# Performance work log

Measured on AMD Instinct MI355X. Metric: run time of the kernel, lower is better.

Reference implementation:

```python
import math
import jax, jax.numpy as jnp
import numpy as np

B, N, C, H = 64, 197, 768, 12
KEEP_RATE = 0.7

def setup_inputs() -> dict:
    key = jax.random.key(0)
    k0, k1, k2 = jax.random.split(key, 3)
    x = jax.random.normal(k0, (B, N, C), jnp.float32)
    qkv_w = jax.random.normal(k1, (C, 3 * C), jnp.float32) * 0.02
    qkv_b = jnp.zeros((3 * C,), jnp.float32)
    proj_w = jax.random.normal(k2, (C, C), jnp.float32) * 0.02
    proj_b = jnp.zeros((C,), jnp.float32)
    return {"x": x, "qkv_w": qkv_w, "qkv_b": qkv_b, "proj_w": proj_w, "proj_b": proj_b}

def reference(x, qkv_w, qkv_b, proj_w, proj_b):
    b, n, c = x.shape
    d = c // H
    scale = d ** -0.5
    # qkv: [B,N,3C] -> [3,B,H,N,d]
    qkv = (x @ qkv_w + qkv_b).reshape(b, n, 3, H, d)
    qkv = jnp.transpose(qkv, (2, 0, 3, 1, 4))
    q, k, v = qkv[0], qkv[1], qkv[2]
    attn = jax.nn.softmax(jnp.einsum('bhnd,bhmd->bhnm', q, k) * scale, axis=-1)  # [B,H,N,N]
    out = jnp.einsum('bhnm,bhmd->bhnd', attn, v)          # [B,H,N,d]
    out = jnp.transpose(out, (0, 2, 1, 3)).reshape(b, n, c)
    x_out = out @ proj_w + proj_b                          # [B,N,C]
    # dynamic token pruning via CLS attention (row 0, excluding CLS itself)
    left_tokens = math.ceil(KEEP_RATE * (n - 1))
    cls_attn = attn[:, :, 0, 1:].mean(axis=1)              # [B,N-1]
    _, idx = jax.lax.top_k(cls_attn, left_tokens)          # descending, sorted
    index = jnp.broadcast_to(idx[:, :, None], (b, left_tokens, c))
    return (x_out, index, idx, cls_attn, left_tokens)
```

## Files before the change

kernel.cpp:

```cpp
#include <hip/hip_runtime.h>
#include <math.h>

#define BB   64
#define NTOK 197
#define CC   768
#define HH   12
#define DH   64
#define MTOT (BB * NTOK)
#define MPAD 12672
#define LEFT 138

#define XOUT_OFF  0
#define INDEX_OFF 9682944
#define IDX_OFF   16465920
#define CLS_OFF   16474752
#define LT_OFF    16487296

typedef short s8v __attribute__((ext_vector_type(8)));
typedef short s4v __attribute__((ext_vector_type(4)));
typedef float f4v __attribute__((ext_vector_type(4)));

#define GLOAD16(g, l) __builtin_amdgcn_global_load_lds( \
    (const __attribute__((address_space(1))) unsigned int*)(g), \
    (__attribute__((address_space(3))) unsigned int*)(l), 16, 0, 0)

__device__ __forceinline__ unsigned short f2bf(float f) {
    union { float f; unsigned int i; } x; x.f = f;
    unsigned int r = x.i + 0x7FFFu + ((x.i >> 16) & 1u);
    return (unsigned short)(r >> 16);
}

__global__ __launch_bounds__(256)
void convert_x(const float* __restrict__ in, unsigned short* __restrict__ outb)
{
    size_t i = ((size_t)blockIdx.x * 256 + threadIdx.x) * 8;
    float4 a = *(const float4*)(in + i);
    float4 b = *(const float4*)(in + i + 4);
    s8v r;
    r[0] = (short)f2bf(a.x); r[1] = (short)f2bf(a.y);
    r[2] = (short)f2bf(a.z); r[3] = (short)f2bf(a.w);
    r[4] = (short)f2bf(b.x); r[5] = (short)f2bf(b.y);
    r[6] = (short)f2bf(b.z); r[7] = (short)f2bf(b.w);
    *(s8v*)(outb + i) = r;
}

__global__ __launch_bounds__(256)
void transpose_w(const float* __restrict__ in, unsigned short* __restrict__ outb, int N)
{
    __shared__ float tile[32][33];
    const int bi = blockIdx.x, bj = blockIdx.y;
    const int tx = threadIdx.x & 31, ty = threadIdx.x >> 5;
#pragma unroll
    for (int r = ty; r < 32; r += 8)
        tile[r][tx] = in[(size_t)(bi * 32 + r) * N + bj * 32 + tx];
    __syncthreads();
#pragma unroll
    for (int r = ty; r < 32; r += 8)
        outb[(size_t)(bj * 32 + r) * 768 + bi * 32 + tx] = f2bf(tile[tx][r]);
}

__global__ __launch_bounds__(256, 3)
void gemm_bf16(const unsigned short* __restrict__ A, const unsigned short* __restrict__ BT,
               const float* __restrict__ bias, int ncolt, int mode,
               unsigned short* __restrict__ outb, float* __restrict__ outf)
{
    const int id = blockIdx.x;
    const int xcd = id & 7;
    const int t = id >> 3;
    const int ct = t % ncolt, s = t / ncolt;
    const int rt = s * 8 + xcd;
    if (rt >= 99) return;
    const int m0 = rt * 128, n0 = ct * 128;

    const int tid = threadIdx.x;
    const int wave = tid >> 6, lane = tid & 63;
    const int quad = lane >> 4, l16 = lane & 15;
    const int rowbase = (wave >> 1) * 64, colbase = (wave & 1) * 64;
    __shared__ __align__(16) short As[128 * 64];
    __shared__ __align__(16) short Bs[128 * 64];

    const int rA   = lane >> 3;
    const int gcol = ((lane & 7) ^ rA) * 8;
    unsigned int agof[4], bgof[4];
#pragma unroll
    for (int i = 0; i < 4; ++i) {
        int c = wave * 4 + i;
        agof[i] = (unsigned int)((m0 + c * 8 + rA) * 768 + gcol);
        bgof[i] = (unsigned int)((n0 + c * 8 + rA) * 768 + gcol);
    }
    int aoff[4], boff[4];
#pragma unroll
    for (int i = 0; i < 4; ++i) {
        aoff[i] = (rowbase + i * 16 + l16) * 64 + ((quad ^ (l16 & 7)) * 8);
        boff[i] = (colbase + i * 16 + l16) * 64 + ((quad ^ (l16 & 7)) * 8);
    }

    f4v acc[4][4];
#pragma unroll
    for (int i = 0; i < 4; ++i)
#pragma unroll
        for (int j = 0; j < 4; ++j) acc[i][j] = (f4v)0.f;

    for (int k0 = 0; k0 < 768; k0 += 64) {
#pragma unroll
        for (int i = 0; i < 4; ++i) {
            int c = wave * 4 + i;
            GLOAD16(A  + agof[i] + k0, &As[c * 512]);
            GLOAD16(BT + bgof[i] + k0, &Bs[c * 512]);
        }
        __syncthreads();
#pragma unroll
        for (int ks = 0; ks < 2; ++ks) {
            const int x = ks * 32;
            s8v af[4], bf[4];
#pragma unroll
            for (int i = 0; i < 4; ++i) af[i] = *(const s8v*)&As[aoff[i] ^ x];
#pragma unroll
            for (int j = 0; j < 4; ++j) bf[j] = *(const s8v*)&Bs[boff[j] ^ x];
#pragma unroll
            for (int i = 0; i < 4; ++i)
#pragma unroll
                for (int j = 0; j < 4; ++j)
                    acc[i][j] = __builtin_amdgcn_mfma_f32_16x16x32_bf16(bf[j], af[i], acc[i][j], 0, 0, 0);
        }
        __syncthreads();
    }

    const int ncols = mode ? 768 : 2304;
#pragma unroll
    for (int i = 0; i < 4; ++i) {
        const int m = m0 + rowbase + i * 16 + l16;
        if (m >= MTOT) continue;
#pragma unroll
        for (int j = 0; j < 4; ++j) {
            const int nb = n0 + colbase + j * 16 + quad * 4;
            float4 b4 = *(const float4*)&bias[nb];
            if (mode == 1) {
                float4 r;
                r.x = acc[i][j][0] + b4.x; r.y = acc[i][j][1] + b4.y;
                r.z = acc[i][j][2] + b4.z; r.w = acc[i][j][3] + b4.w;
                *(float4*)(outf + (size_t)m * ncols + nb) = r;
            } else {
                s4v r;
                r[0] = (short)f2bf(acc[i][j][0] + b4.x);
                r[1] = (short)f2bf(acc[i][j][1] + b4.y);
                r[2] = (short)f2bf(acc[i][j][2] + b4.z);
                r[3] = (short)f2bf(acc[i][j][3] + b4.w);
                *(s4v*)(outb + (size_t)m * ncols + nb) = r;
            }
        }
    }
}

#define PSTR 226
#define AW   5
#define ATH  320

__global__ __launch_bounds__(ATH)
void attn_mfma(const unsigned short* __restrict__ qkv, unsigned short* __restrict__ attnbf)
{
    const int bh = blockIdx.x;
    const int b = bh / HH, h = bh - b * HH;
    const int tid = threadIdx.x;
    const int wave = tid >> 6, lane = tid & 63;
    const int quad = lane >> 4, l16 = lane & 15;
    __shared__ short Vs[64 * PSTR];
    __shared__ short Ps[AW][16 * PSTR];

    const unsigned short* qg = qkv + (size_t)b * NTOK * 2304 + h * DH;
    const unsigned short* kg = qg + 768;
    const unsigned short* vg = qg + 1536;

    if (tid < NTOK) {
#pragma unroll
        for (int c = 0; c < 8; ++c) {
            s8v vv = *(const s8v*)(vg + (size_t)tid * 2304 + c * 8);
#pragma unroll
            for (int e = 0; e < 8; ++e) Vs[(c * 8 + e) * PSTR + tid] = vv[e];
        }
    }
    for (int f = tid; f < 64 * (PSTR - NTOK); f += ATH) {
        int dd = f / (PSTR - NTOK);
        int tk = NTOK + (f - dd * (PSTR - NTOK));
        Vs[dd * PSTR + tk] = 0;
    }
    __syncthreads();

    for (int strip = wave; strip < 13; strip += AW) {
        const int mq = min(strip * 16 + l16, NTOK - 1);
        const s8v aq0 = *(const s8v*)(qg + (size_t)mq * 2304 + quad * 8);
        const s8v aq1 = *(const s8v*)(qg + (size_t)mq * 2304 + 32 + quad * 8);

        f4v sacc[14];
#pragma unroll
        for (int j = 0; j < 14; ++j) sacc[j] = (f4v)0.f;
#pragma unroll
        for (int j = 0; j < 14; ++j) {
            const int kt = min(j * 16 + l16, NTOK - 1);
            s8v bk0 = *(const s8v*)(kg + (size_t)kt * 2304 + quad * 8);
            s8v bk1 = *(const s8v*)(kg + (size_t)kt * 2304 + 32 + quad * 8);
            sacc[j] = __builtin_amdgcn_mfma_f32_16x16x32_bf16(bk0, aq0, sacc[j], 0, 0, 0);
            sacc[j] = __builtin_amdgcn_mfma_f32_16x16x32_bf16(bk1, aq1, sacc[j], 0, 0, 0);
        }

        float mx = -1e30f;
#pragma unroll
        for (int j = 0; j < 14; ++j)
#pragma unroll
            for (int r = 0; r < 4; ++r) {
                const int key = j * 16 + quad * 4 + r;
                float s = (key < NTOK) ? sacc[j][r] * 0.125f : -1e30f;
                sacc[j][r] = s;
                mx = fmaxf(mx, s);
            }
        mx = fmaxf(mx, __shfl_xor(mx, 16, 64));
        mx = fmaxf(mx, __shfl_xor(mx, 32, 64));

        float sm = 0.f;
#pragma unroll
        for (int j = 0; j < 14; ++j) {
            s4v pk;
#pragma unroll
            for (int r = 0; r < 4; ++r) {
                const int key = j * 16 + quad * 4 + r;
                float p = (key < NTOK) ? __expf(sacc[j][r] - mx) : 0.f;
                sm += p;
                pk[r] = (short)f2bf(p);
            }
            *(s4v*)&Ps[wave][l16 * PSTR + j * 16 + quad * 4] = pk;
        }
        sm += __shfl_xor(sm, 16, 64);
        sm += __shfl_xor(sm, 32, 64);
        const float rcp = 1.f / sm;

        f4v oacc[4];
#pragma unroll
        for (int j = 0; j < 4; ++j) oacc[j] = (f4v)0.f;
#pragma unroll
        for (int t = 0; t < 7; ++t) {
            const int ko = t * 32 + quad * 8;
            s8v ap = *(const s8v*)&Ps[wave][l16 * PSTR + ko];
#pragma unroll
            for (int j = 0; j < 4; ++j) {
                s8v bv = *(const s8v*)&Vs[(j * 16 + l16) * PSTR + ko];
                oacc[j] = __builtin_amdgcn_mfma_f32_16x16x32_bf16(bv, ap, oacc[j], 0, 0, 0);
            }
        }
        const int qrow = strip * 16 + l16;
        if (qrow < NTOK) {
#pragma unroll
            for (int j = 0; j < 4; ++j) {
                s4v o4;
#pragma unroll
                for (int r = 0; r < 4; ++r) o4[r] = (short)f2bf(oacc[j][r] * rcp);
                *(s4v*)&attnbf[((size_t)b * NTOK + qrow) * 768 + h * DH + j * 16 + quad * 4] = o4;
            }
        }
    }
}

#define QCH 64

__global__ __launch_bounds__(256)
void qr_kernel(const float* __restrict__ x, const float* __restrict__ qkv_w,
               const float* __restrict__ qkv_b, float* __restrict__ rws,
               float* __restrict__ bconst)
{
    const int blk = blockIdx.x;
    const int b = blk / HH, h = blk - b * HH;
    const int tid = threadIdx.x;
    __shared__ float x0[CC];
    __shared__ float q0h[DH];
    __shared__ float wbuf[2][QCH * DH];
    for (int c = tid; c < CC; c += 256) x0[c] = x[(size_t)b * NTOK * CC + c];
    for (int u = tid; u < QCH * DH; u += 256) {
        int cc = u >> 6, o = u & 63;
        wbuf[0][u] = qkv_w[(size_t)cc * 2304 + h * DH + o];
    }
    __syncthreads();
    float acc = 0.f;
    if (tid < DH) acc = qkv_b[h * DH + tid];
    for (int k = 0; k < CC / QCH; ++k) {
        const int cur = k & 1;
        if (k + 1 < CC / QCH) {
            const int cbase = (k + 1) * QCH;
            for (int u = tid; u < QCH * DH; u += 256) {
                int cc = u >> 6, o = u & 63;
                wbuf[cur ^ 1][u] = qkv_w[(size_t)(cbase + cc) * 2304 + h * DH + o];
            }
        }
        if (tid < DH) {
            const int cbase = k * QCH;
#pragma unroll
            for (int cc = 0; cc < QCH; ++cc)
                acc = fmaf(x0[cbase + cc], wbuf[cur][cc * 64 + tid], acc);
        }
        __syncthreads();
    }
    if (tid < DH) q0h[tid] = acc;
    __syncthreads();
    for (int c = tid; c < CC; c += 256) {
        const float* wrow = qkv_w + (size_t)c * 2304 + CC + h * DH;
        float acc2 = 0.f;
#pragma unroll
        for (int d = 0; d < DH; d += 4) {
            float4 w4 = *(const float4*)(wrow + d);
            acc2 = fmaf(w4.x, q0h[d + 0], acc2);
            acc2 = fmaf(w4.y, q0h[d + 1], acc2);
            acc2 = fmaf(w4.z, q0h[d + 2], acc2);
            acc2 = fmaf(w4.w, q0h[d + 3], acc2);
        }
        rws[((size_t)b * HH + h) * CC + c] = acc2;
    }
    if (tid == 0) {
        float acc3 = 0.f;
        for (int d = 0; d < DH; ++d) acc3 += q0h[d] * qkv_b[CC + h * DH + d];
        bconst[blk] = acc3;
    }
}

__global__ __launch_bounds__(256)
void cls_s(const float* __restrict__ x, const float* __restrict__ rws,
           const float* __restrict__ bconst, float* __restrict__ sws)
{
    const int b = blockIdx.y;
    const int tid = threadIdx.x;
    __shared__ __align__(16) float rl[HH * 772];
    __shared__ float bcs[HH];
#pragma unroll
    for (int h = 0; h < HH; ++h)
        for (int c = tid; c < CC; c += 256)
            rl[h * 772 + c] = rws[((size_t)b * HH + h) * CC + c];
    if (tid < HH) bcs[tid] = bconst[b * HH + tid];
    __syncthreads();
    const int local = blockIdx.x * 256 + tid;
    if (local < NTOK * HH) {
        const int tok = local / HH;
        const int h = local - tok * HH;
        const float* xr = x + ((size_t)b * NTOK + tok) * CC;
        const float* rp = rl + h * 772;
        float acc = 0.f;
#pragma unroll 8
        for (int c = 0; c < CC; c += 4) {
            float4 x4 = *(const float4*)(xr + c);
            float4 r4 = *(const float4*)(rp + c);
            acc = fmaf(x4.x, r4.x, acc);
            acc = fmaf(x4.y, r4.y, acc);
            acc = fmaf(x4.z, r4.z, acc);
            acc = fmaf(x4.w, r4.w, acc);
        }
        sws[((size_t)b * HH + h) * NTOK + tok] = (acc + bcs[h]) * 0.125f;
    }
}

__global__ __launch_bounds__(256)
void cls_topk(const float* __restrict__ sws, float* __restrict__ out, int write_lt)
{
    const int b = blockIdx.x, tid = threadIdx.x;
    const int wave = tid >> 6, lane = tid & 63;
    __shared__ float sbuf[HH][208];
    __shared__ float pm[4][208];
    __shared__ float vals[256];
    __shared__ int   idxs[256];

    for (int jj = lane; jj < 208; jj += 64) pm[wave][jj] = 0.f;
    if (tid < NTOK) {
#pragma unroll
        for (int h = 0; h < HH; ++h)
            sbuf[h][tid] = sws[((size_t)b * HH + h) * NTOK + tid];
    }
    __syncthreads();

    for (int h = wave; h < HH; h += 4) {
        float sv[4], ev[4];
        float mx = -1e30f;
#pragma unroll
        for (int t = 0; t < 4; ++t) {
            int j = lane + 64 * t;
            sv[t] = (j < NTOK) ? sbuf[h][j] : -1e30f;
            mx = fmaxf(mx, sv[t]);
        }
#pragma unroll
        for (int off = 1; off < 64; off <<= 1) mx = fmaxf(mx, __shfl_xor(mx, off, 64));
        float sm = 0.f;
#pragma unroll
        for (int t = 0; t < 4; ++t) {
            int j = lane + 64 * t;
            ev[t] = (j < NTOK) ? expf(sv[t] - mx) : 0.f;
            sm += ev[t];
        }
#pragma unroll
        for (int off = 1; off < 64; off <<= 1) sm += __shfl_xor(sm, off, 64);
#pragma unroll
        for (int t = 0; t < 4; ++t) {
            int j = lane + 64 * t;
            if (j < NTOK) pm[wave][j] += ev[t] / sm;
        }
    }
    __syncthreads();

    float v = -INFINITY;
    int id = 256 + tid;
    if (tid < NTOK - 1) {
        int j = tid + 1;
        float s = ((pm[0][j] + pm[1][j]) + (pm[2][j] + pm[3][j])) * (1.f / 12.f);
        v = s; id = tid;
        out[CLS_OFF + (size_t)b * (NTOK - 1) + tid] = s;
    }
    vals[tid] = v; idxs[tid] = id;
    __syncthreads();

    for (int k = 2; k <= 256; k <<= 1) {
        for (int j = k >> 1; j > 0; j >>= 1) {
            int ixj = tid ^ j;
            if (ixj > tid) {
                float va = vals[tid], vb2 = vals[ixj];
                int ia = idxs[tid], ib = idxs[ixj];
                bool aLess = (va > vb2) || (va == vb2 && ia < ib);
                bool dir = ((tid & k) == 0);
                if (dir != aLess) {
                    vals[tid] = vb2; vals[ixj] = va;
                    idxs[tid] = ib;  idxs[ixj] = ia;
                }
            }
            __syncthreads();
        }
    }

    if (tid < LEFT) out[IDX_OFF + (size_t)b * LEFT + tid] = (float)idxs[tid];
    if (write_lt && b == 0 && tid == 0) out[LT_OFF] = (float)LEFT;
}

__global__ __launch_bounds__(64)
void write_index(const float* __restrict__ idx_in, float* __restrict__ out)
{
    const int row = blockIdx.x;
    const float v = idx_in[row];
    const int tid = threadIdx.x;
    float4 r; r.x = v; r.y = v; r.z = v; r.w = v;
#pragma unroll
    for (int i = 0; i < 3; ++i)
        *(float4*)(out + INDEX_OFF + (size_t)row * CC + (tid + 64 * i) * 4) = r;
}

extern "C" void kernel_launch(void* const* d_in, const int* in_sizes, int n_in,
                              void* d_out, int out_size, void* d_ws, size_t ws_size,
                              hipStream_t stream)
{
    const float* x      = (const float*)d_in[0];
    const float* qkv_w  = (const float*)d_in[1];
    const float* qkv_b  = (const float*)d_in[2];
    const float* proj_w = (const float*)d_in[3];
    const float* proj_b = (const float*)d_in[4];
    float* out = (float*)d_out;

    char* w = (char*)d_ws;
    unsigned short* xbf   = (unsigned short*)w; w += (size_t)MPAD * CC * 2;
    unsigned short* wt1   = (unsigned short*)w; w += (size_t)3 * CC * CC * 2;
    unsigned short* wt2   = (unsigned short*)w; w += (size_t)CC * CC * 2;
    unsigned short* qkvbf = (unsigned short*)w; w += (size_t)MTOT * 3 * CC * 2;
    unsigned short* atbf  = (unsigned short*)w; w += (size_t)MPAD * CC * 2;
    float* rws    = (float*)w; w += (size_t)BB * HH * CC * 4;
    float* bconst = (float*)w; w += (size_t)BB * HH * 4;
    float* sws    = (float*)w; w += (size_t)BB * HH * NTOK * 4;

    convert_x<<<dim3(4728), 256, 0, stream>>>(x, xbf);
    transpose_w<<<dim3(24, 72), 256, 0, stream>>>(qkv_w, wt1, 3 * CC);
    transpose_w<<<dim3(24, 24), 256, 0, stream>>>(proj_w, wt2, CC);
    qr_kernel<<<dim3(BB * HH), 256, 0, stream>>>(x, qkv_w, qkv_b, rws, bconst);
    cls_s<<<dim3(10, 64), 256, 0, stream>>>(x, rws, bconst, sws);
    cls_topk<<<dim3(BB), 256, 0, stream>>>(sws, out, (out_size > LT_OFF) ? 1 : 0);
    write_index<<<dim3(BB * LEFT), 64, 0, stream>>>(out + IDX_OFF, out);
    gemm_bf16<<<dim3(8 * 18 * 13), 256, 0, stream>>>(xbf, wt1, qkv_b, 18, 0, qkvbf, nullptr);
    attn_mfma<<<dim3(BB * HH), ATH, 0, stream>>>(qkvbf, atbf);
    gemm_bf16<<<dim3(8 * 6 * 13), 256, 0, stream>>>(atbf, wt2, proj_b, 6, 1,
                                                    nullptr, out + XOUT_OFF);
}
```

Measured before the change: 337.5 us.

## Batch eight samples per block in CLS query kernel to reuse weights

The CLS-query projection kernel now processes a group of eight batch elements per block instead of one, so each weight tile loaded into shared memory and each K-weight row read from global memory is reused across eight samples. All 256 threads now do work in the first phase, where previously only 64 were active. The grid shrinks from 768 blocks to 96, which lowers parallelism, and shared-memory use per block grows.

```diff
diff --git a/kernel.cpp b/kernel.cpp
--- a/kernel.cpp
+++ b/kernel.cpp
@@ -259,63 +259,83 @@
     }
 }
 
-#define QCH 64
+#define QCH  64
+#define BGRP 8
 
 __global__ __launch_bounds__(256)
 void qr_kernel(const float* __restrict__ x, const float* __restrict__ qkv_w,
                const float* __restrict__ qkv_b, float* __restrict__ rws,
                float* __restrict__ bconst)
 {
-    const int blk = blockIdx.x;
-    const int b = blk / HH, h = blk - b * HH;
+    const int h  = blockIdx.x;
+    const int b0 = blockIdx.y * BGRP;
     const int tid = threadIdx.x;
-    __shared__ float x0[CC];
-    __shared__ float q0h[DH];
+    __shared__ float x0s[BGRP][CC];
     __shared__ float wbuf[2][QCH * DH];
-    for (int c = tid; c < CC; c += 256) x0[c] = x[(size_t)b * NTOK * CC + c];
+    __shared__ float q0s[BGRP][DH];
+
+    for (int u = tid; u < BGRP * CC; u += 256) {
+        int b = u / CC, c = u - b * CC;
+        x0s[b][c] = x[(size_t)(b0 + b) * NTOK * CC + c];
+    }
     for (int u = tid; u < QCH * DH; u += 256) {
-        int cc = u >> 6, o = u & 63;
-        wbuf[0][u] = qkv_w[(size_t)cc * 2304 + h * DH + o];
-    }
-    __syncthreads();
-    float acc = 0.f;
-    if (tid < DH) acc = qkv_b[h * DH + tid];
+        int cc = u >> 6, dd = u & 63;
+        wbuf[0][u] = qkv_w[(size_t)cc * 2304 + h * DH + dd];
+    }
+    __syncthreads();
+
+    const int d  = tid & 63;
+    const int bA = tid >> 6;
+    const int bB = bA + 4;
+    float accA = qkv_b[h * DH + d];
+    float accB = qkv_b[h * DH + d];
     for (int k = 0; k < CC / QCH; ++k) {
         const int cur = k & 1;
         if (k + 1 < CC / QCH) {
             const int cbase = (k + 1) * QCH;
             for (int u = tid; u < QCH * DH; u += 256) {
-                int cc = u >> 6, o = u & 63;
-                wbuf[cur ^ 1][u] = qkv_w[(size_t)(cbase + cc) * 2304 + h * DH + o];
-            }
-        }
-        if (tid < DH) {
-            const int cbase = k * QCH;
-#pragma unroll
-            for (int cc = 0; cc < QCH; ++cc)
-                acc = fmaf(x0[cbase + cc], wbuf[cur][cc * 64 + tid], acc);
+                int cc = u >> 6, dd = u & 63;
+                wbuf[cur ^ 1][u] = qkv_w[(size_t)(cbase + cc) * 2304 + h * DH + dd];
+            }
+        }
+        const int cb = k * QCH;
+#pragma unroll
+        for (int cc = 0; cc < QCH; ++cc) {
+            const float wv = wbuf[cur][cc * 64 + d];
+            accA = fmaf(x0s[bA][cb + cc], wv, accA);
+            accB = fmaf(x0s[bB][cb + cc], wv, accB);
         }
         __syncthreads();
     }
-    if (tid < DH) q0h[tid] = acc;
-    __syncthreads();
+    q0s[bA][d] = accA;
+    q0s[bB][d] = accB;
+    __syncthreads();
+
+    if (tid < BGRP) {
+        float acc3 = 0.f;
+        for (int dd = 0; dd < DH; ++dd) acc3 += q0s[tid][dd] * qkv_b[CC + h * DH + dd];
+        bconst[(b0 + tid) * HH + h] = acc3;
+    }
+
     for (int c = tid; c < CC; c += 256) {
         const float* wrow = qkv_w + (size_t)c * 2304 + CC + h * DH;
-        float acc2 = 0.f;
-#pragma unroll
-        for (int d = 0; d < DH; d += 4) {
-            float4 w4 = *(const float4*)(wrow + d);
-            acc2 = fmaf(w4.x, q0h[d + 0], acc2);
-            acc2 = fmaf(w4.y, q0h[d + 1], acc2);
-            acc2 = fmaf(w4.z, q0h[d + 2], acc2);
-            acc2 = fmaf(w4.w, q0h[d + 3], acc2);
-        }
-        rws[((size_t)b * HH + h) * CC + c] = acc2;
-    }
-    if (tid == 0) {
-        float acc3 = 0.f;
-        for (int d = 0; d < DH; ++d) acc3 += q0h[d] * qkv_b[CC + h * DH + d];
-        bconst[blk] = acc3;
+        float acc2[BGRP];
+#pragma unroll
+        for (int b = 0; b < BGRP; ++b) acc2[b] = 0.f;
+#pragma unroll
+        for (int dd = 0; dd < DH; dd += 4) {
+            float4 w4 = *(const float4*)(wrow + dd);
+#pragma unroll
+            for (int b = 0; b < BGRP; ++b) {
+                acc2[b] = fmaf(w4.x, q0s[b][dd + 0], acc2[b]);
+                acc2[b] = fmaf(w4.y, q0s[b][dd + 1], acc2[b]);
+                acc2[b] = fmaf(w4.z, q0s[b][dd + 2], acc2[b]);
+                acc2[b] = fmaf(w4.w, q0s[b][dd + 3], acc2[b]);
+            }
+        }
+#pragma unroll
+        for (int b = 0; b < BGRP; ++b)
+            rws[((size_t)(b0 + b) * HH + h) * CC + c] = acc2[b];
     }
 }
 
@@ -467,7 +487,7 @@
     convert_x<<<dim3(4728), 256, 0, stream>>>(x, xbf);
     transpose_w<<<dim3(24, 72), 256, 0, stream>>>(qkv_w, wt1, 3 * CC);
     transpose_w<<<dim3(24, 24), 256, 0, stream>>>(proj_w, wt2, CC);
-    qr_kernel<<<dim3(BB * HH), 256, 0, stream>>>(x, qkv_w, qkv_b, rws, bconst);
+    qr_kernel<<<dim3(HH, BB / BGRP), 256, 0, stream>>>(x, qkv_w, qkv_b, rws, bconst);
     cls_s<<<dim3(10, 64), 256, 0, stream>>>(x, rws, bconst, sws);
     cls_topk<<<dim3(BB), 256, 0, stream>>>(sws, out, (out_size > LT_OFF) ? 1 : 0);
     write_index<<<dim3(BB * LEFT), 64, 0, stream>>>(out + IDX_OFF, out);
```

Result: slower. 344.7 us (+2.1%).
